# Performance work log

Hardware: AMD Instinct MI355X
Metric: run time of the kernel (lower is better)

Reference implementation:

```python
import jax, jax.numpy as jnp
import numpy as np

B, T, CV, DIM = 1, 1024, 8, 2048
NH, HD, W = 32, 64, 8
BMM = NH * HD


def swa_transform(x, window):
    # x: (b, t, cv, d) -> (b, t, window*cv, d)
    # matches torch pad-front + unfold + transpose + reshape: window-major, char-minor
    b, t, cv, d = x.shape
    xp = jnp.pad(x, ((0, 0), (window - 1, 0), (0, 0), (0, 0)))
    wins = jnp.stack([xp[:, w:w + t] for w in range(window)], axis=2)  # (b,t,W,cv,d)
    return wins.reshape(b, t, window * cv, d)


def rope(x, freqs):
    # interleaved-pair RoPE (rotary_embedding_torch default, theta=10000)
    # x: (..., hd); freqs broadcastable against x[..., 0::2]
    cos, sin = jnp.cos(freqs), jnp.sin(freqs)
    x1, x2 = x[..., 0::2], x[..., 1::2]
    return jnp.stack([x1 * cos - x2 * sin, x1 * sin + x2 * cos], axis=-1).reshape(x.shape)


def setup_inputs() -> dict:
    key = jax.random.key(0)
    ks = jax.random.split(key, 6)
    s = 0.02
    return {
        "x": jax.random.normal(ks[0], (B, T, DIM), dtype=jnp.float32),
        "chars": jax.random.normal(ks[1], (B, T, CV, DIM), dtype=jnp.float32),
        "wq": jax.random.normal(ks[2], (BMM, DIM), dtype=jnp.float32) * s,
        "wk": jax.random.normal(ks[3], (BMM, DIM), dtype=jnp.float32) * s,
        "wv": jax.random.normal(ks[4], (BMM, DIM), dtype=jnp.float32) * s,
        "wo": jax.random.normal(ks[5], (DIM, BMM), dtype=jnp.float32) * s,
    }


def reference(x, chars, wq, wk, wv, wo):
    b, t = x.shape[0], x.shape[1]
    cv = chars.shape[2]
    wc = W * cv

    q = x @ wq.T                     # (b, t, BMM)
    k = chars @ wk.T                 # (b, t, cv, BMM)
    v = chars @ wv.T

    k = swa_transform(k, W)          # (b, t, W*cv, BMM)
    v = swa_transform(v, W)

    q = q.reshape(b, t, NH, HD).transpose(0, 2, 1, 3)          # (b, nh, t, hd)
    k = k.reshape(b, t, wc, NH, HD).transpose(0, 3, 1, 2, 4)   # (b, nh, t, wc, hd)
    v = v.reshape(b, t, wc, NH, HD).transpose(0, 3, 1, 2, 4)   # (b, nh, t, wc, hd)

    inv_freq = 1.0 / (10000.0 ** (jnp.arange(0, HD, 2, dtype=jnp.float32) / HD))
    freqs = jnp.arange(t, dtype=jnp.float32)[:, None] * inv_freq  # (t, hd/2)

    q = rope(q, freqs)                       # rotate over token axis (-2)
    k = rope(k, freqs[:, None, :])           # rotate over token axis (-3), broadcast over window

    scores = jnp.einsum('bhtd,bhtkd->bhtk', q, k) / np.float32(np.sqrt(HD))
    attn = jax.nn.softmax(scores, axis=-1)   # (b, nh, t, wc)
    out = jnp.einsum('bhtk,bhtkd->bhtd', attn, v)
    out = out.transpose(0, 2, 1, 3).reshape(b, t, NH * HD)
    return out @ wo.T
```

## Files before the change

kernel.cpp:

```cpp
#include <hip/hip_runtime.h>
#include <hip/hip_bf16.h>
#include <cstdint>
#include <cstddef>

static constexpr int kT   = 1024;
static constexpr int kCV  = 8;
static constexpr int kDim = 2048;
static constexpr int kNH  = 32;
static constexpr int kHD  = 64;
static constexpr int kW   = 8;
static constexpr int kK   = 2048;

using bf16_t = __hip_bfloat16;

typedef __attribute__((ext_vector_type(8))) __bf16 bf16x8;
typedef __attribute__((ext_vector_type(4))) float  f32x4;

__device__ __forceinline__ float bf_bits_to_f32(unsigned short u) {
    union { unsigned int i; float f; } c;
    c.i = ((unsigned int)u) << 16;
    return c.f;
}

struct CastArgs {
    const float* src[6];
    bf16_t*      dst[6];
    int          cum[7];
};

__global__ void cast_all(CastArgs a, int total_chunks) {
    const int c = blockIdx.x * blockDim.x + threadIdx.x;
    if (c >= total_chunks) return;
    int r = 0;
#pragma unroll
    for (int i = 1; i <= 5; ++i) r += (c >= a.cum[i]) ? 1 : 0;
    const int local = c - a.cum[r];
    const float* s = a.src[r] + (size_t)local * 8;
    bf16_t*      d = a.dst[r] + (size_t)local * 8;
    const float4 lo = *reinterpret_cast<const float4*>(s);
    const float4 hi = *reinterpret_cast<const float4*>(s + 4);
    union { bf16_t h[8]; uint4 u; } o;
    o.h[0] = __float2bfloat16(lo.x); o.h[1] = __float2bfloat16(lo.y);
    o.h[2] = __float2bfloat16(lo.z); o.h[3] = __float2bfloat16(lo.w);
    o.h[4] = __float2bfloat16(hi.x); o.h[5] = __float2bfloat16(hi.y);
    o.h[6] = __float2bfloat16(hi.z); o.h[7] = __float2bfloat16(hi.w);
    *reinterpret_cast<uint4*>(d) = o.u;
}

template <bool OUT_BF16, typename CT>
__device__ __forceinline__ void gemm_body(const bf16_t* __restrict__ A,
                                          const bf16_t* __restrict__ Wt,
                                          CT* __restrict__ C,
                                          int bm, int bn, int ldc) {
    __shared__ bf16_t As[128 * 64];
    __shared__ bf16_t Bs[128 * 64];

    const int tid  = threadIdx.x;
    const int wave = tid >> 6;
    const int lane = tid & 63;
    const int l16  = lane & 15;
    const int quad = lane >> 4;
    const int wm   = (wave >> 1) * 64;
    const int wn   = (wave & 1) * 64;

    f32x4 acc[4][4];
#pragma unroll
    for (int i = 0; i < 4; ++i)
#pragma unroll
        for (int j = 0; j < 4; ++j) acc[i][j] = (f32x4)0.0f;

    const int srow = tid >> 3;
    const int jg   = (tid & 7) ^ (srow & 7);
    const bf16_t* gA = A  + (size_t)(bm + srow) * kK + jg * 8;
    const bf16_t* gB = Wt + (size_t)(bn + srow) * kK + jg * 8;

    for (int k0 = 0; k0 < kK; k0 += 64) {
#pragma unroll
        for (int i = 0; i < 4; ++i) {
            __builtin_amdgcn_global_load_lds(
                (const __attribute__((address_space(1))) void*)(gA + (size_t)i * 32 * kK + k0),
                (__attribute__((address_space(3))) void*)(As + i * 2048 + wave * 512),
                16, 0, 0);
            __builtin_amdgcn_global_load_lds(
                (const __attribute__((address_space(1))) void*)(gB + (size_t)i * 32 * kK + k0),
                (__attribute__((address_space(3))) void*)(Bs + i * 2048 + wave * 512),
                16, 0, 0);
        }
        __syncthreads();

#pragma unroll
        for (int ph = 0; ph < 2; ++ph) {
            bf16x8 af[4], bfr[4];
#pragma unroll
            for (int i = 0; i < 4; ++i) {
                const int jla = (ph * 4 + quad) ^ (l16 & 7);
                af[i]  = *reinterpret_cast<const bf16x8*>(
                    &As[(wm + i * 16 + l16) * 64 + jla * 8]);
                bfr[i] = *reinterpret_cast<const bf16x8*>(
                    &Bs[(wn + i * 16 + l16) * 64 + jla * 8]);
            }
#pragma unroll
            for (int i = 0; i < 4; ++i)
#pragma unroll
                for (int j = 0; j < 4; ++j)
                    acc[i][j] = __builtin_amdgcn_mfma_f32_16x16x32_bf16(
                        af[i], bfr[j], acc[i][j], 0, 0, 0);
        }
        __syncthreads();
    }

#pragma unroll
    for (int i = 0; i < 4; ++i) {
#pragma unroll
        for (int rr = 0; rr < 4; ++rr) {
            const int row = bm + wm + i * 16 + quad * 4 + rr;
#pragma unroll
            for (int j = 0; j < 4; ++j) {
                const int col = bn + wn + j * 16 + l16;
                if constexpr (OUT_BF16) {
                    C[(size_t)row * ldc + col] = __float2bfloat16(acc[i][j][rr]);
                } else {
                    C[(size_t)row * ldc + col] = acc[i][j][rr];
                }
            }
        }
    }
}

__global__ __launch_bounds__(256, 3) void proj_kernel(
    const bf16_t* __restrict__ xb, const bf16_t* __restrict__ cb,
    const bf16_t* __restrict__ wqb, const bf16_t* __restrict__ wkvb,
    bf16_t* __restrict__ qb, bf16_t* __restrict__ kvb) {
    const int bid = blockIdx.x;
    if (bid < 2048) {
        const int bm = (bid >> 5) * 128;
        const int bn = (bid & 31) * 128;
        gemm_body<true>(cb, wkvb, kvb, bm, bn, 4096);
    } else {
        const int t  = bid - 2048;
        const int bm = (t >> 4) * 128;
        const int bn = (t & 15) * 128;
        gemm_body<true>(xb, wqb, qb, bm, bn, 2048);
    }
}

__global__ __launch_bounds__(256, 3) void out_gemm(
    const bf16_t* __restrict__ ob, const bf16_t* __restrict__ wob,
    float* __restrict__ out) {
    const int bm = (blockIdx.x >> 4) * 128;
    const int bn = (blockIdx.x & 15) * 128;
    gemm_body<false>(ob, wob, out, bm, bn, 2048);
}

static constexpr int kTT   = 16;
static constexpr int kSRC  = kTT + kW - 1;
static constexpr int kROWS = kSRC * kCV;
static constexpr int kLDK  = 72;

__global__ __launch_bounds__(1024) void attn_kernel(
    const bf16_t* __restrict__ qb,
    const bf16_t* __restrict__ kvb,
    bf16_t* __restrict__ ob) {
    __shared__ unsigned short kl[kROWS * kLDK];
    __shared__ unsigned short vl[kROWS * kLDK];
    __shared__ float ql[kTT * 64];
    __shared__ float al[kTT * 64];

    const int t0   = blockIdx.x * kTT;
    const int h    = blockIdx.y;
    const int tid  = threadIdx.x;
    const int wave = tid >> 6;
    const int lane = tid & 63;

    ql[tid] = __bfloat162float(qb[(size_t)(t0 + wave) * kDim + h * kHD + lane]);

    const long long grow0 = (long long)(t0 - (kW - 1)) * kCV;
#pragma unroll
    for (int c = tid; c < kROWS * 8; c += 1024) {
        const int r   = c >> 3;
        const int sub = c & 7;
        const long long grow = grow0 + r;
        uint4 kd = make_uint4(0, 0, 0, 0), vd = make_uint4(0, 0, 0, 0);
        if (grow >= 0) {
            const size_t gb = (size_t)grow * 4096 + h * kHD + sub * 8;
            kd = *reinterpret_cast<const uint4*>(kvb + gb);
            vd = *reinterpret_cast<const uint4*>(kvb + gb + 2048);
        }
        *reinterpret_cast<uint4*>(&kl[r * kLDK + sub * 8]) = kd;
        *reinterpret_cast<uint4*>(&vl[r * kLDK + sub * 8]) = vd;
    }
    __syncthreads();

    const int r = wave * kCV + lane;
    float s = 0.0f;
#pragma unroll
    for (int c = 0; c < 8; ++c) {
        union { uint4 u; unsigned short us[8]; } kv;
        kv.u = *reinterpret_cast<const uint4*>(&kl[r * kLDK + c * 8]);
        const float4 qa = *reinterpret_cast<const float4*>(&ql[wave * 64 + c * 8]);
        const float4 qc = *reinterpret_cast<const float4*>(&ql[wave * 64 + c * 8 + 4]);
        s += bf_bits_to_f32(kv.us[0]) * qa.x + bf_bits_to_f32(kv.us[1]) * qa.y +
             bf_bits_to_f32(kv.us[2]) * qa.z + bf_bits_to_f32(kv.us[3]) * qa.w +
             bf_bits_to_f32(kv.us[4]) * qc.x + bf_bits_to_f32(kv.us[5]) * qc.y +
             bf_bits_to_f32(kv.us[6]) * qc.z + bf_bits_to_f32(kv.us[7]) * qc.w;
    }
    s *= 0.125f;

    float m = s;
#pragma unroll
    for (int off = 32; off; off >>= 1) m = fmaxf(m, __shfl_xor(m, off));
    const float e = __expf(s - m);
    float sum = e;
#pragma unroll
    for (int off = 32; off; off >>= 1) sum += __shfl_xor(sum, off);
    al[wave * 64 + lane] = e / sum;

    float o = 0.0f;
#pragma unroll
    for (int k2 = 0; k2 < 64; ++k2)
        o += al[wave * 64 + k2] * bf_bits_to_f32(vl[(wave * kCV + k2) * kLDK + lane]);
    ob[(size_t)(t0 + wave) * kDim + h * kHD + lane] = __float2bfloat16(o);
}

extern "C" void kernel_launch(void* const* d_in, const int* in_sizes, int n_in,
                              void* d_out, int out_size, void* d_ws,
                              size_t ws_size, hipStream_t stream) {
    const float* x     = (const float*)d_in[0];
    const float* chars = (const float*)d_in[1];
    const float* wq    = (const float*)d_in[2];
    const float* wk    = (const float*)d_in[3];
    const float* wv    = (const float*)d_in[4];
    const float* wo    = (const float*)d_in[5];
    float* out = (float*)d_out;

    char* p = (char*)d_ws;
    bf16_t* xb   = (bf16_t*)p; p += (size_t)kT * kDim * 2;
    bf16_t* cb   = (bf16_t*)p; p += (size_t)kT * kCV * kDim * 2;
    bf16_t* wqb  = (bf16_t*)p; p += (size_t)kDim * kDim * 2;
    bf16_t* wkvb = (bf16_t*)p; p += (size_t)2 * kDim * kDim * 2;
    bf16_t* wob  = (bf16_t*)p; p += (size_t)kDim * kDim * 2;
    bf16_t* qb   = (bf16_t*)p; p += (size_t)kT * kDim * 2;
    bf16_t* kvb  = (bf16_t*)p; p += (size_t)kT * kCV * 2 * kDim * 2;
    bf16_t* ob   = (bf16_t*)p; p += (size_t)kT * kDim * 2;

    CastArgs ca;
    ca.src[0] = x;     ca.dst[0] = xb;
    ca.src[1] = chars; ca.dst[1] = cb;
    ca.src[2] = wq;    ca.dst[2] = wqb;
    ca.src[3] = wk;    ca.dst[3] = wkvb;
    ca.src[4] = wv;    ca.dst[4] = wkvb + (size_t)kDim * kDim;
    ca.src[5] = wo;    ca.dst[5] = wob;
    const int sizes[6] = {kT * kDim, kT * kCV * kDim, kDim * kDim,
                          kDim * kDim, kDim * kDim, kDim * kDim};
    int cum = 0;
    ca.cum[0] = 0;
    for (int i = 0; i < 6; ++i) { cum += sizes[i] / 8; ca.cum[i + 1] = cum; }
    cast_all<<<dim3((cum + 255) / 256), dim3(256), 0, stream>>>(ca, cum);

    proj_kernel<<<dim3(2176), dim3(256), 0, stream>>>(xb, cb, wqb, wkvb, qb, kvb);

    attn_kernel<<<dim3(kT / kTT, kNH), dim3(1024), 0, stream>>>(qb, kvb, ob);

    out_gemm<<<dim3(128), dim3(256), 0, stream>>>(ob, wob, out);
}
```

Before: 360.5 us.

## Split-K the output GEMM with atomics and vectorize attention PV reads

The output projection GEMM now splits K into two halves over 256 blocks instead of 128, accumulating into a zero-initialized fp32 output with atomicAdd. The aim is to fill more of the device's compute units. The attention PV product now reads 8 bf16 values per lane as a vector from LDS and reduces partial sums across key groups with shuffles, replacing scalar LDS reads. The cost is an extra memset, atomic traffic on the output, and non-deterministic summation order.

```diff
diff --git a/kernel.cpp b/kernel.cpp
--- a/kernel.cpp
+++ b/kernel.cpp
@@ -47,11 +47,12 @@
     *reinterpret_cast<uint4*>(d) = o.u;
 }
 
-template <bool OUT_BF16, typename CT>
+template <int EPI, typename CT>
 __device__ __forceinline__ void gemm_body(const bf16_t* __restrict__ A,
                                           const bf16_t* __restrict__ Wt,
                                           CT* __restrict__ C,
-                                          int bm, int bn, int ldc) {
+                                          int bm, int bn, int ldc,
+                                          int kb, int ke) {
     __shared__ bf16_t As[128 * 64];
     __shared__ bf16_t Bs[128 * 64];
 
@@ -74,7 +75,7 @@
     const bf16_t* gA = A  + (size_t)(bm + srow) * kK + jg * 8;
     const bf16_t* gB = Wt + (size_t)(bn + srow) * kK + jg * 8;
 
-    for (int k0 = 0; k0 < kK; k0 += 64) {
+    for (int k0 = kb; k0 < ke; k0 += 64) {
 #pragma unroll
         for (int i = 0; i < 4; ++i) {
             __builtin_amdgcn_global_load_lds(
@@ -117,10 +118,10 @@
 #pragma unroll
             for (int j = 0; j < 4; ++j) {
                 const int col = bn + wn + j * 16 + l16;
-                if constexpr (OUT_BF16) {
+                if constexpr (EPI == 1) {
                     C[(size_t)row * ldc + col] = __float2bfloat16(acc[i][j][rr]);
                 } else {
-                    C[(size_t)row * ldc + col] = acc[i][j][rr];
+                    atomicAdd((float*)&C[(size_t)row * ldc + col], acc[i][j][rr]);
                 }
             }
         }
@@ -135,21 +136,23 @@
     if (bid < 2048) {
         const int bm = (bid >> 5) * 128;
         const int bn = (bid & 31) * 128;
-        gemm_body<true>(cb, wkvb, kvb, bm, bn, 4096);
+        gemm_body<1>(cb, wkvb, kvb, bm, bn, 4096, 0, kK);
     } else {
         const int t  = bid - 2048;
         const int bm = (t >> 4) * 128;
         const int bn = (t & 15) * 128;
-        gemm_body<true>(xb, wqb, qb, bm, bn, 2048);
+        gemm_body<1>(xb, wqb, qb, bm, bn, 2048, 0, kK);
     }
 }
 
 __global__ __launch_bounds__(256, 3) void out_gemm(
     const bf16_t* __restrict__ ob, const bf16_t* __restrict__ wob,
     float* __restrict__ out) {
-    const int bm = (blockIdx.x >> 4) * 128;
-    const int bn = (blockIdx.x & 15) * 128;
-    gemm_body<false>(ob, wob, out, bm, bn, 2048);
+    const int ks = blockIdx.x >> 7;
+    const int t  = blockIdx.x & 127;
+    const int bm = (t >> 4) * 128;
+    const int bn = (t & 15) * 128;
+    gemm_body<2>(ob, wob, out, bm, bn, 2048, ks * 1024, ks * 1024 + 1024);
 }
 
 static constexpr int kTT   = 16;
@@ -175,7 +178,6 @@
     ql[tid] = __bfloat162float(qb[(size_t)(t0 + wave) * kDim + h * kHD + lane]);
 
     const long long grow0 = (long long)(t0 - (kW - 1)) * kCV;
-#pragma unroll
     for (int c = tid; c < kROWS * 8; c += 1024) {
         const int r   = c >> 3;
         const int sub = c & 7;
@@ -215,11 +217,33 @@
     for (int off = 32; off; off >>= 1) sum += __shfl_xor(sum, off);
     al[wave * 64 + lane] = e / sum;
 
-    float o = 0.0f;
-#pragma unroll
-    for (int k2 = 0; k2 < 64; ++k2)
-        o += al[wave * 64 + k2] * bf_bits_to_f32(vl[(wave * kCV + k2) * kLDK + lane]);
-    ob[(size_t)(t0 + wave) * kDim + h * kHD + lane] = __float2bfloat16(o);
+    const int kg = lane >> 3;
+    const int dg = lane & 7;
+    float acc8[8];
+#pragma unroll
+    for (int i = 0; i < 8; ++i) acc8[i] = 0.0f;
+#pragma unroll
+    for (int j = 0; j < 8; ++j) {
+        const int key = kg * 8 + j;
+        const int rr  = wave * kCV + key;
+        union { uint4 u; unsigned short us[8]; } vv;
+        vv.u = *reinterpret_cast<const uint4*>(&vl[rr * kLDK + dg * 8]);
+        const float p = al[wave * 64 + key];
+#pragma unroll
+        for (int i = 0; i < 8; ++i) acc8[i] += p * bf_bits_to_f32(vv.us[i]);
+    }
+#pragma unroll
+    for (int off = 8; off <= 32; off <<= 1)
+#pragma unroll
+        for (int i = 0; i < 8; ++i) acc8[i] += __shfl_xor(acc8[i], off);
+
+    if (kg == 0) {
+        union { bf16_t hh[8]; uint4 u; } o;
+#pragma unroll
+        for (int i = 0; i < 8; ++i) o.hh[i] = __float2bfloat16(acc8[i]);
+        *reinterpret_cast<uint4*>(
+            &ob[(size_t)(t0 + wave) * kDim + h * kHD + dg * 8]) = o.u;
+    }
 }
 
 extern "C" void kernel_launch(void* const* d_in, const int* in_sizes, int n_in,
@@ -257,9 +281,11 @@
     for (int i = 0; i < 6; ++i) { cum += sizes[i] / 8; ca.cum[i + 1] = cum; }
     cast_all<<<dim3((cum + 255) / 256), dim3(256), 0, stream>>>(ca, cum);
 
+    hipMemsetAsync(out, 0, (size_t)kT * kDim * sizeof(float), stream);
+
     proj_kernel<<<dim3(2176), dim3(256), 0, stream>>>(xb, cb, wqb, wkvb, qb, kvb);
 
     attn_kernel<<<dim3(kT / kTT, kNH), dim3(1024), 0, stream>>>(qb, kvb, ob);
 
-    out_gemm<<<dim3(128), dim3(256), 0, stream>>>(ob, wob, out);
-}
+    out_gemm<<<dim3(256), dim3(256), 0, stream>>>(ob, wob, out);
+}
```

Result: no change. 366.1 us (+1.5%).

## Rewrite windowed attention as one wave per token-head with register-resident K/V

Applied to the files above, without the earlier changes.

The attention kernel no longer stages a shared-memory tile of K/V for 16 tokens per 1024-thread block. Each 64-lane wave now handles one (token, head) pair and loads its 64 window rows directly from global memory into registers. Scores, softmax and the weighted V sum are reduced with lane shuffles. This removes the LDS staging and block-wide barrier, but gives up the reuse of overlapping window rows between neighbouring tokens, so global/L2 traffic for K/V rises roughly by the window factor.

```diff
diff --git a/kernel.cpp b/kernel.cpp
--- a/kernel.cpp
+++ b/kernel.cpp
@@ -152,74 +152,85 @@
     gemm_body<false>(ob, wob, out, bm, bn, 2048);
 }
 
-static constexpr int kTT   = 16;
-static constexpr int kSRC  = kTT + kW - 1;
-static constexpr int kROWS = kSRC * kCV;
-static constexpr int kLDK  = 72;
-
-__global__ __launch_bounds__(1024) void attn_kernel(
+__global__ __launch_bounds__(256) void attn_kernel(
     const bf16_t* __restrict__ qb,
     const bf16_t* __restrict__ kvb,
     bf16_t* __restrict__ ob) {
-    __shared__ unsigned short kl[kROWS * kLDK];
-    __shared__ unsigned short vl[kROWS * kLDK];
-    __shared__ float ql[kTT * 64];
-    __shared__ float al[kTT * 64];
-
-    const int t0   = blockIdx.x * kTT;
-    const int h    = blockIdx.y;
-    const int tid  = threadIdx.x;
-    const int wave = tid >> 6;
-    const int lane = tid & 63;
-
-    ql[tid] = __bfloat162float(qb[(size_t)(t0 + wave) * kDim + h * kHD + lane]);
-
-    const long long grow0 = (long long)(t0 - (kW - 1)) * kCV;
-#pragma unroll
-    for (int c = tid; c < kROWS * 8; c += 1024) {
-        const int r   = c >> 3;
-        const int sub = c & 7;
-        const long long grow = grow0 + r;
-        uint4 kd = make_uint4(0, 0, 0, 0), vd = make_uint4(0, 0, 0, 0);
-        if (grow >= 0) {
-            const size_t gb = (size_t)grow * 4096 + h * kHD + sub * 8;
-            kd = *reinterpret_cast<const uint4*>(kvb + gb);
-            vd = *reinterpret_cast<const uint4*>(kvb + gb + 2048);
-        }
-        *reinterpret_cast<uint4*>(&kl[r * kLDK + sub * 8]) = kd;
-        *reinterpret_cast<uint4*>(&vl[r * kLDK + sub * 8]) = vd;
-    }
-    __syncthreads();
-
-    const int r = wave * kCV + lane;
-    float s = 0.0f;
-#pragma unroll
-    for (int c = 0; c < 8; ++c) {
-        union { uint4 u; unsigned short us[8]; } kv;
-        kv.u = *reinterpret_cast<const uint4*>(&kl[r * kLDK + c * 8]);
-        const float4 qa = *reinterpret_cast<const float4*>(&ql[wave * 64 + c * 8]);
-        const float4 qc = *reinterpret_cast<const float4*>(&ql[wave * 64 + c * 8 + 4]);
-        s += bf_bits_to_f32(kv.us[0]) * qa.x + bf_bits_to_f32(kv.us[1]) * qa.y +
-             bf_bits_to_f32(kv.us[2]) * qa.z + bf_bits_to_f32(kv.us[3]) * qa.w +
-             bf_bits_to_f32(kv.us[4]) * qc.x + bf_bits_to_f32(kv.us[5]) * qc.y +
-             bf_bits_to_f32(kv.us[6]) * qc.z + bf_bits_to_f32(kv.us[7]) * qc.w;
-    }
-    s *= 0.125f;
-
-    float m = s;
-#pragma unroll
-    for (int off = 32; off; off >>= 1) m = fmaxf(m, __shfl_xor(m, off));
-    const float e = __expf(s - m);
-    float sum = e;
-#pragma unroll
-    for (int off = 32; off; off >>= 1) sum += __shfl_xor(sum, off);
-    al[wave * 64 + lane] = e / sum;
-
-    float o = 0.0f;
-#pragma unroll
-    for (int k2 = 0; k2 < 64; ++k2)
-        o += al[wave * 64 + k2] * bf_bits_to_f32(vl[(wave * kCV + k2) * kLDK + lane]);
-    ob[(size_t)(t0 + wave) * kDim + h * kHD + lane] = __float2bfloat16(o);
+    const int wid  = (blockIdx.x * 256 + threadIdx.x) >> 6;
+    const int t    = wid >> 5;
+    const int h    = wid & 31;
+    const int lane = threadIdx.x & 63;
+    const int kg   = lane >> 3;
+    const int dg   = lane & 7;
+
+    const int  st    = t - (kW - 1) + kg;
+    const bool valid = (st >= 0);
+
+    union { uint4 u; unsigned short us[8]; } qu;
+    qu.u = *reinterpret_cast<const uint4*>(qb + (size_t)t * kDim + h * kHD + dg * 8);
+    float qf[8];
+#pragma unroll
+    for (int i = 0; i < 8; ++i) qf[i] = bf_bits_to_f32(qu.us[i]);
+
+    const size_t base =
+        (size_t)(valid ? st : 0) * (size_t)(kCV * 4096) + h * kHD + dg * 8;
+    union { uint4 u; unsigned short us[8]; } kr[8], vr[8];
+#pragma unroll
+    for (int j = 0; j < 8; ++j) {
+        const size_t a = base + (size_t)j * 4096;
+        kr[j].u = valid ? *reinterpret_cast<const uint4*>(kvb + a)
+                        : make_uint4(0, 0, 0, 0);
+        vr[j].u = valid ? *reinterpret_cast<const uint4*>(kvb + a + 2048)
+                        : make_uint4(0, 0, 0, 0);
+    }
+
+    float s[8];
+#pragma unroll
+    for (int j = 0; j < 8; ++j) {
+        float acc = 0.0f;
+#pragma unroll
+        for (int i = 0; i < 8; ++i) acc += qf[i] * bf_bits_to_f32(kr[j].us[i]);
+        s[j] = acc;
+    }
+#pragma unroll
+    for (int off = 1; off <= 4; off <<= 1)
+#pragma unroll
+        for (int j = 0; j < 8; ++j) s[j] += __shfl_xor(s[j], off);
+#pragma unroll
+    for (int j = 0; j < 8; ++j) s[j] *= 0.125f;
+
+    float m = s[0];
+#pragma unroll
+    for (int j = 1; j < 8; ++j) m = fmaxf(m, s[j]);
+#pragma unroll
+    for (int off = 8; off <= 32; off <<= 1) m = fmaxf(m, __shfl_xor(m, off));
+    float e[8], sum = 0.0f;
+#pragma unroll
+    for (int j = 0; j < 8; ++j) { e[j] = __expf(s[j] - m); sum += e[j]; }
+#pragma unroll
+    for (int off = 8; off <= 32; off <<= 1) sum += __shfl_xor(sum, off);
+    const float inv = 1.0f / sum;
+
+    float o[8];
+#pragma unroll
+    for (int i = 0; i < 8; ++i) o[i] = 0.0f;
+#pragma unroll
+    for (int j = 0; j < 8; ++j) {
+        const float p = e[j] * inv;
+#pragma unroll
+        for (int i = 0; i < 8; ++i) o[i] += p * bf_bits_to_f32(vr[j].us[i]);
+    }
+#pragma unroll
+    for (int off = 8; off <= 32; off <<= 1)
+#pragma unroll
+        for (int i = 0; i < 8; ++i) o[i] += __shfl_xor(o[i], off);
+
+    if (kg == 0) {
+        union { bf16_t hh[8]; uint4 u; } ov;
+#pragma unroll
+        for (int i = 0; i < 8; ++i) ov.hh[i] = __float2bfloat16(o[i]);
+        *reinterpret_cast<uint4*>(&ob[(size_t)t * kDim + h * kHD + dg * 8]) = ov.u;
+    }
 }
 
 extern "C" void kernel_launch(void* const* d_in, const int* in_sizes, int n_in,
@@ -259,7 +270,7 @@
 
     proj_kernel<<<dim3(2176), dim3(256), 0, stream>>>(xb, cb, wqb, wkvb, qb, kvb);
 
-    attn_kernel<<<dim3(kT / kTT, kNH), dim3(1024), 0, stream>>>(qb, kvb, ob);
+    attn_kernel<<<dim3(kT * kNH / 4), dim3(256), 0, stream>>>(qb, kvb, ob);
 
     out_gemm<<<dim3(128), dim3(256), 0, stream>>>(ob, wob, out);
 }
```

New measurement: 365.2 us. About the same (+1.3%).
